# Performance work log

Measured on AMD Instinct MI355X. Metric: run time of the kernel, lower is better.

Reference implementation:

```python
import jax, jax.numpy as jnp
import numpy as np

BN_EPS = 1e-5


def setup_inputs() -> dict:
    key = jax.random.key(0)
    k_x, k_w, k_g, k_b, k_m, k_v = jax.random.split(key, 6)
    B, P, C = 8, 512, 1024
    x = jax.random.normal(k_x, (B, P, C), dtype=jnp.float32)
    # Linear(dim, dim, bias=False) weight, torch layout (out, in)
    W_qkv = jax.random.normal(k_w, (C, C), dtype=jnp.float32) * (1.0 / np.sqrt(C))
    # BatchNorm1d(dim) eval-mode params over channel axis
    bn_gamma = jnp.ones((C,), jnp.float32) + 0.01 * jax.random.normal(k_g, (C,), dtype=jnp.float32)
    bn_beta = 0.01 * jax.random.normal(k_b, (C,), dtype=jnp.float32)
    bn_mean = 0.01 * jax.random.normal(k_m, (C,), dtype=jnp.float32)
    bn_var = jnp.abs(1.0 + 0.01 * jax.random.normal(k_v, (C,), dtype=jnp.float32))
    gra_sharp = jnp.float32(2.0)
    return {"x": x, "W_qkv": W_qkv, "bn_gamma": bn_gamma, "bn_beta": bn_beta,
            "bn_mean": bn_mean, "bn_var": bn_var, "gra_sharp": gra_sharp}


def reference(x, W_qkv, bn_gamma, bn_beta, bn_mean, bn_var, gra_sharp):
    B, P, C = x.shape
    H = 8  # num_heads
    Wd = P // H  # per-head token width (heads split the SEQUENCE axis)

    # shared Linear(dim,dim,bias=False); q = k = v since same module on same x
    qkv = jnp.einsum('bpc,dc->bpd', x, W_qkv)          # (B, P, C)
    qkv = qkv.transpose(0, 2, 1)                        # (B, C, P)
    # BatchNorm1d(dim), eval mode: normalize channel axis (dim=1)
    inv = jax.lax.rsqrt(bn_var + BN_EPS)
    qkv = (qkv - bn_mean[None, :, None]) * (inv * bn_gamma)[None, :, None] + bn_beta[None, :, None]

    # split_last((H, -1)) on seq axis then transpose(1,2): (B, H, C, Wd)
    q = qkv.reshape(B, C, H, Wd).transpose(0, 2, 1, 3)
    k = q
    v = q

    # channel-by-channel scores per head: (B, H, C, C)
    scores = jnp.einsum('bhcw,bhdw->bhcd', q, k) / gra_sharp
    # NON-STANDARD: softmax over the HEAD axis (dim=1); dropout = identity (eval)
    attn = jax.nn.softmax(scores, axis=1)

    h = jnp.einsum('bhcd,bhdw->bhcw', attn, v)          # (B, H, C, Wd)
    h = h.transpose(0, 2, 1, 3).reshape(B, C, P)        # merge heads back into P
    h = h.transpose(0, 2, 1)                            # (B, P, C)
    return h, attn
```

## Files before the change

### kernel.cpp

```cpp
#include <hip/hip_runtime.h>
#include <math.h>

#define B 8
#define P 512
#define C 1024
#define H 8
#define WD 64
#define BN_EPS 1e-5f

typedef __attribute__((ext_vector_type(8))) __bf16 bf16x8;
typedef __attribute__((ext_vector_type(4))) __bf16 bf16x4;
typedef __attribute__((ext_vector_type(4))) float f32x4;

__global__ __launch_bounds__(256) void split_hi_lo(
    const float* __restrict__ x, const float* __restrict__ Wq,
    __bf16* __restrict__ xhi, __bf16* __restrict__ xlo,
    __bf16* __restrict__ whi, __bf16* __restrict__ wlo)
{
    const size_t NX4 = (size_t)B * P * C / 4;
    size_t idx = (size_t)blockIdx.x * 256 + threadIdx.x;
    float4 v;
    __bf16 *dh, *dl;
    size_t o;
    if (idx < NX4) {
        v = ((const float4*)x)[idx];
        dh = xhi; dl = xlo; o = idx * 4;
    } else {
        v = ((const float4*)Wq)[idx - NX4];
        dh = whi; dl = wlo; o = (idx - NX4) * 4;
    }
    float f[4] = {v.x, v.y, v.z, v.w};
    bf16x4 hv, lv;
    #pragma unroll
    for (int j = 0; j < 4; ++j) {
        __bf16 hb = (__bf16)f[j];
        hv[j] = hb;
        lv[j] = (__bf16)(f[j] - (float)hb);
    }
    *(bf16x4*)&dh[o] = hv;
    *(bf16x4*)&dl[o] = lv;
}

__global__ __launch_bounds__(256) void qkv_bn_mfma(
    const __bf16* __restrict__ xhi, const __bf16* __restrict__ xlo,
    const __bf16* __restrict__ whi, const __bf16* __restrict__ wlo,
    const float* __restrict__ gamma, const float* __restrict__ beta,
    const float* __restrict__ mean, const float* __restrict__ var,
    __bf16* __restrict__ Yhi, __bf16* __restrict__ Ylo, __bf16* __restrict__ Zhi)
{
    const int dt = blockIdx.x;
    const int pt = blockIdx.y;
    const int b  = blockIdx.z;
    const int t = threadIdx.x, lane = t & 63, wid = t >> 6;
    const int quadd = (wid >> 1) * 32, quadp = (wid & 1) * 32;
    const int lr = lane & 15, lk = (lane >> 4) * 8;

    const int drow0 = dt * 64 + quadd + lr;
    const size_t xrow0 = ((size_t)b * P + pt * 64 + quadp + lr) * C;

    f32x4 acc[2][2];
    #pragma unroll
    for (int tm = 0; tm < 2; ++tm)
        #pragma unroll
        for (int tn = 0; tn < 2; ++tn)
            acc[tm][tn] = (f32x4){0.f, 0.f, 0.f, 0.f};

    for (int c0 = 0; c0 < C; c0 += 32) {
        const int col = c0 + lk;
        bf16x8 ah[2], al[2], bh[2], bl[2];
        #pragma unroll
        for (int tm = 0; tm < 2; ++tm) {
            size_t ia = (size_t)(drow0 + tm * 16) * C + col;
            ah[tm] = *(const bf16x8*)&whi[ia];
            al[tm] = *(const bf16x8*)&wlo[ia];
        }
        #pragma unroll
        for (int tn = 0; tn < 2; ++tn) {
            size_t ib = xrow0 + (size_t)tn * 16 * C + col;
            bh[tn] = *(const bf16x8*)&xhi[ib];
            bl[tn] = *(const bf16x8*)&xlo[ib];
        }
        #pragma unroll
        for (int tm = 0; tm < 2; ++tm)
            #pragma unroll
            for (int tn = 0; tn < 2; ++tn) {
                acc[tm][tn] = __builtin_amdgcn_mfma_f32_16x16x32_bf16(ah[tm], bh[tn], acc[tm][tn], 0, 0, 0);
                acc[tm][tn] = __builtin_amdgcn_mfma_f32_16x16x32_bf16(ah[tm], bl[tn], acc[tm][tn], 0, 0, 0);
                acc[tm][tn] = __builtin_amdgcn_mfma_f32_16x16x32_bf16(al[tm], bh[tn], acc[tm][tn], 0, 0, 0);
            }
    }

    const int rgrp = (lane >> 4) * 4;
    #pragma unroll
    for (int tm = 0; tm < 2; ++tm) {
        const int dbase = dt * 64 + quadd + tm * 16 + rgrp;
        float4 g4 = *(const float4*)&gamma[dbase];
        float4 bb4 = *(const float4*)&beta[dbase];
        float4 m4 = *(const float4*)&mean[dbase];
        float4 v4 = *(const float4*)&var[dbase];
        float gf[4] = {g4.x, g4.y, g4.z, g4.w};
        float bf[4] = {bb4.x, bb4.y, bb4.z, bb4.w};
        float mf[4] = {m4.x, m4.y, m4.z, m4.w};
        float vf[4] = {v4.x, v4.y, v4.z, v4.w};
        float sc[4];
        #pragma unroll
        for (int r = 0; r < 4; ++r) sc[r] = rsqrtf(vf[r] + BN_EPS) * gf[r];

        #pragma unroll
        for (int tn = 0; tn < 2; ++tn) {
            const int p = pt * 64 + quadp + tn * 16 + lr;
            bf16x4 zq;
            #pragma unroll
            for (int r = 0; r < 4; ++r) {
                float n = (acc[tm][tn][r] - mf[r]) * sc[r] + bf[r];
                __bf16 hb = (__bf16)n;
                __bf16 lb = (__bf16)(n - (float)hb);
                size_t yi = ((size_t)b * C + dbase + r) * P + p;
                Yhi[yi] = hb;
                Ylo[yi] = lb;
                zq[r] = hb;
            }
            *(bf16x4*)&Zhi[((size_t)b * P + p) * C + dbase] = zq;
        }
    }
}

__global__ __launch_bounds__(256) void scores_softmax_mfma(
    const __bf16* __restrict__ Yhi, const __bf16* __restrict__ Ylo,
    const float* __restrict__ gs_ptr, float* __restrict__ attn)
{
    const int ct = blockIdx.x, dt = blockIdx.y, b = blockIdx.z;
    const int t = threadIdx.x, lane = t & 63, wid = t >> 6;
    const int quadc = (wid >> 1) * 32, quadd = (wid & 1) * 32;
    const int lr = lane & 15, lk = (lane >> 4) * 8;
    const float scale = 1.0f / gs_ptr[0];

    const size_t rowc = (size_t)b * C + ct * 64 + quadc + lr;
    const size_t rowd = (size_t)b * C + dt * 64 + quadd + lr;

    f32x4 acc[8][2][2];
    #pragma unroll
    for (int h = 0; h < H; ++h)
        #pragma unroll
        for (int tm = 0; tm < 2; ++tm)
            #pragma unroll
            for (int tn = 0; tn < 2; ++tn)
                acc[h][tm][tn] = (f32x4){0.f, 0.f, 0.f, 0.f};

    #pragma unroll
    for (int h = 0; h < H; ++h) {
        #pragma unroll
        for (int s = 0; s < 2; ++s) {
            const int col = h * 64 + s * 32 + lk;
            bf16x8 ah[2], al[2], bh[2], bl[2];
            #pragma unroll
            for (int tm = 0; tm < 2; ++tm) {
                size_t ia = (rowc + tm * 16) * P + col;
                ah[tm] = *(const bf16x8*)&Yhi[ia];
                al[tm] = *(const bf16x8*)&Ylo[ia];
                size_t ib = (rowd + tm * 16) * P + col;
                bh[tm] = *(const bf16x8*)&Yhi[ib];
                bl[tm] = *(const bf16x8*)&Ylo[ib];
            }
            #pragma unroll
            for (int tm = 0; tm < 2; ++tm)
                #pragma unroll
                for (int tn = 0; tn < 2; ++tn) {
                    acc[h][tm][tn] = __builtin_amdgcn_mfma_f32_16x16x32_bf16(ah[tm], bh[tn], acc[h][tm][tn], 0, 0, 0);
                    acc[h][tm][tn] = __builtin_amdgcn_mfma_f32_16x16x32_bf16(ah[tm], bl[tn], acc[h][tm][tn], 0, 0, 0);
                    acc[h][tm][tn] = __builtin_amdgcn_mfma_f32_16x16x32_bf16(al[tm], bh[tn], acc[h][tm][tn], 0, 0, 0);
                }
        }
    }

    #pragma unroll
    for (int tm = 0; tm < 2; ++tm)
        #pragma unroll
        for (int tn = 0; tn < 2; ++tn)
            #pragma unroll
            for (int r = 0; r < 4; ++r) {
                float v[8];
                float m = -1e30f;
                #pragma unroll
                for (int h = 0; h < H; ++h) {
                    v[h] = acc[h][tm][tn][r] * scale;
                    m = fmaxf(m, v[h]);
                }
                float ssum = 0.f;
                #pragma unroll
                for (int h = 0; h < H; ++h) { v[h] = __expf(v[h] - m); ssum += v[h]; }
                float inv = 1.0f / ssum;
                #pragma unroll
                for (int h = 0; h < H; ++h) acc[h][tm][tn][r] = v[h] * inv;
            }

    #pragma unroll
    for (int h = 0; h < H; ++h) {
        #pragma unroll
        for (int tm = 0; tm < 2; ++tm) {
            const int c = ct * 64 + quadc + tm * 16 + (lane >> 4) * 4;
            #pragma unroll
            for (int tn = 0; tn < 2; ++tn) {
                const int d = dt * 64 + quadd + tn * 16 + lr;
                float* op = attn + (((size_t)(b * H + h) * C + c) * C + d);
                #pragma unroll
                for (int r = 0; r < 4; ++r) op[(size_t)r * C] = acc[h][tm][tn][r];
            }
        }
    }
}

__global__ __launch_bounds__(256) void pv_mfma(
    const float* __restrict__ attn, const __bf16* __restrict__ Zhi,
    float* __restrict__ out0)
{
    const int ct = blockIdx.x;
    const int bh = blockIdx.y;
    const int b = bh >> 3, h = bh & 7;
    const int t = threadIdx.x, lane = t & 63, wid = t >> 6;
    const int quadc = (wid >> 1) * 64;
    const int quadw = (wid & 1) * 32;
    const int lr = lane & 15, lk = (lane >> 4) * 8;

    __shared__ __bf16 Ah[128 * 64];
    __shared__ __bf16 Al[128 * 64];

    const float* Ab = attn + ((size_t)bh * C + (size_t)ct * 128) * C;

    f32x4 acc[4][2];
    #pragma unroll
    for (int tm = 0; tm < 4; ++tm)
        #pragma unroll
        for (int tn = 0; tn < 2; ++tn)
            acc[tm][tn] = (f32x4){0.f, 0.f, 0.f, 0.f};

    const int sr  = t >> 4;
    const int scb = (t & 15) * 4;

    for (int d0 = 0; d0 < C; d0 += 64) {
        #pragma unroll
        for (int q = 0; q < 8; ++q) {
            int rr = sr + q * 16;
            float4 v = *(const float4*)&Ab[(size_t)rr * C + d0 + scb];
            __bf16 h0 = (__bf16)v.x, h1 = (__bf16)v.y, h2 = (__bf16)v.z, h3 = (__bf16)v.w;
            bf16x4 hq = {h0, h1, h2, h3};
            bf16x4 lq = {(__bf16)(v.x - (float)h0), (__bf16)(v.y - (float)h1),
                         (__bf16)(v.z - (float)h2), (__bf16)(v.w - (float)h3)};
            int off = (rr * 128 + scb * 2) ^ ((rr & 7) << 4);
            *(bf16x4*)((char*)Ah + off) = hq;
            *(bf16x4*)((char*)Al + off) = lq;
        }
        __syncthreads();
        #pragma unroll
        for (int s = 0; s < 2; ++s) {
            const int k0 = s * 32 + lk;
            bf16x8 bv[2];
            #pragma unroll
            for (int tn = 0; tn < 2; ++tn) {
                const int w = quadw + tn * 16 + lr;
                bv[tn] = *(const bf16x8*)&Zhi[((size_t)b * P + h * 64 + w) * C + d0 + k0];
            }
            #pragma unroll
            for (int tm = 0; tm < 4; ++tm) {
                const int row = quadc + tm * 16 + lr;
                const int off = (row * 128 + k0 * 2) ^ ((row & 7) << 4);
                bf16x8 a_h = *(const bf16x8*)((char*)Ah + off);
                bf16x8 a_l = *(const bf16x8*)((char*)Al + off);
                #pragma unroll
                for (int tn = 0; tn < 2; ++tn) {
                    acc[tm][tn] = __builtin_amdgcn_mfma_f32_16x16x32_bf16(a_h, bv[tn], acc[tm][tn], 0, 0, 0);
                    acc[tm][tn] = __builtin_amdgcn_mfma_f32_16x16x32_bf16(a_l, bv[tn], acc[tm][tn], 0, 0, 0);
                }
            }
        }
        __syncthreads();
    }

    #pragma unroll
    for (int tm = 0; tm < 4; ++tm) {
        const int c0 = ct * 128 + quadc + tm * 16 + (lane >> 4) * 4;
        #pragma unroll
        for (int tn = 0; tn < 2; ++tn) {
            const int w = quadw + tn * 16 + lr;
            f32x4 v = acc[tm][tn];
            *(f32x4*)&out0[((size_t)b * P + h * 64 + w) * C + c0] = v;
        }
    }
}

extern "C" void kernel_launch(void* const* d_in, const int* in_sizes, int n_in,
                              void* d_out, int out_size, void* d_ws, size_t ws_size,
                              hipStream_t stream) {
    const float* x     = (const float*)d_in[0];
    const float* Wq    = (const float*)d_in[1];
    const float* gamma = (const float*)d_in[2];
    const float* beta  = (const float*)d_in[3];
    const float* mean  = (const float*)d_in[4];
    const float* var   = (const float*)d_in[5];
    const float* gs    = (const float*)d_in[6];

    float* out0 = (float*)d_out;
    float* attn = (float*)d_out + (size_t)B * P * C;

    const size_t NE = (size_t)B * C * P;
    __bf16* Yhi = (__bf16*)d_ws;
    __bf16* Ylo = Yhi + NE;
    __bf16* Zhi = Ylo + NE;

    const size_t attn_elems = (size_t)B * H * C * C;
    __bf16* S = (__bf16*)(attn + (attn_elems - 5242880));
    __bf16* xhi = S;
    __bf16* xlo = xhi + (size_t)B * P * C;
    __bf16* whi = xlo + (size_t)B * P * C;
    __bf16* wlo = whi + (size_t)C * C;

    split_hi_lo<<<5120, 256, 0, stream>>>(x, Wq, xhi, xlo, whi, wlo);
    qkv_bn_mfma<<<dim3(16, 8, 8), 256, 0, stream>>>(xhi, xlo, whi, wlo,
                                                    gamma, beta, mean, var,
                                                    Yhi, Ylo, Zhi);
    scores_softmax_mfma<<<dim3(16, 16, 8), 256, 0, stream>>>(Yhi, Ylo, gs, attn);
    pv_mfma<<<dim3(8, 64), 256, 0, stream>>>(attn, Zhi, out0);
}
```

Measured before the change: 400.4 us.

## Fuse scores, head-axis softmax and PV product into one kernel

Merges the scores/softmax kernel and the PV kernel into a single kernel. Each block owns a 32-channel slice and loops over all d tiles: it computes the per-head scores, applies the head-axis softmax, writes attn, stages the probabilities as bf16 in LDS, and accumulates PV immediately. This removes the full fp32 re-read of the large attn tensor. The PV product now uses only the bf16 hi part of the probabilities instead of the hi+lo split, trading precision for fewer MFMAs. The grid shrinks to 256 blocks of 512 threads, and the partial sums are reduced across waves through LDS, which lowers occupancy and latency hiding.

```diff
diff --git a/kernel.cpp b/kernel.cpp
--- a/kernel.cpp
+++ b/kernel.cpp
@@ -5,7 +5,6 @@
 #define P 512
 #define C 1024
 #define H 8
-#define WD 64
 #define BN_EPS 1e-5f
 
 typedef __attribute__((ext_vector_type(8))) __bf16 bf16x8;
@@ -125,166 +124,138 @@
     }
 }
 
-__global__ __launch_bounds__(256) void scores_softmax_mfma(
+__global__ __launch_bounds__(512) void attn_fused(
     const __bf16* __restrict__ Yhi, const __bf16* __restrict__ Ylo,
-    const float* __restrict__ gs_ptr, float* __restrict__ attn)
-{
-    const int ct = blockIdx.x, dt = blockIdx.y, b = blockIdx.z;
-    const int t = threadIdx.x, lane = t & 63, wid = t >> 6;
-    const int quadc = (wid >> 1) * 32, quadd = (wid & 1) * 32;
-    const int lr = lane & 15, lk = (lane >> 4) * 8;
-    const float scale = 1.0f / gs_ptr[0];
-
-    const size_t rowc = (size_t)b * C + ct * 64 + quadc + lr;
-    const size_t rowd = (size_t)b * C + dt * 64 + quadd + lr;
-
-    f32x4 acc[8][2][2];
-    #pragma unroll
-    for (int h = 0; h < H; ++h)
-        #pragma unroll
-        for (int tm = 0; tm < 2; ++tm)
-            #pragma unroll
-            for (int tn = 0; tn < 2; ++tn)
-                acc[h][tm][tn] = (f32x4){0.f, 0.f, 0.f, 0.f};
-
-    #pragma unroll
-    for (int h = 0; h < H; ++h) {
-        #pragma unroll
-        for (int s = 0; s < 2; ++s) {
-            const int col = h * 64 + s * 32 + lk;
-            bf16x8 ah[2], al[2], bh[2], bl[2];
-            #pragma unroll
-            for (int tm = 0; tm < 2; ++tm) {
-                size_t ia = (rowc + tm * 16) * P + col;
-                ah[tm] = *(const bf16x8*)&Yhi[ia];
-                al[tm] = *(const bf16x8*)&Ylo[ia];
-                size_t ib = (rowd + tm * 16) * P + col;
-                bh[tm] = *(const bf16x8*)&Yhi[ib];
-                bl[tm] = *(const bf16x8*)&Ylo[ib];
-            }
-            #pragma unroll
-            for (int tm = 0; tm < 2; ++tm)
-                #pragma unroll
-                for (int tn = 0; tn < 2; ++tn) {
-                    acc[h][tm][tn] = __builtin_amdgcn_mfma_f32_16x16x32_bf16(ah[tm], bh[tn], acc[h][tm][tn], 0, 0, 0);
-                    acc[h][tm][tn] = __builtin_amdgcn_mfma_f32_16x16x32_bf16(ah[tm], bl[tn], acc[h][tm][tn], 0, 0, 0);
-                    acc[h][tm][tn] = __builtin_amdgcn_mfma_f32_16x16x32_bf16(al[tm], bh[tn], acc[h][tm][tn], 0, 0, 0);
-                }
-        }
-    }
-
-    #pragma unroll
-    for (int tm = 0; tm < 2; ++tm)
-        #pragma unroll
-        for (int tn = 0; tn < 2; ++tn)
-            #pragma unroll
-            for (int r = 0; r < 4; ++r) {
-                float v[8];
-                float m = -1e30f;
-                #pragma unroll
-                for (int h = 0; h < H; ++h) {
-                    v[h] = acc[h][tm][tn][r] * scale;
-                    m = fmaxf(m, v[h]);
-                }
-                float ssum = 0.f;
-                #pragma unroll
-                for (int h = 0; h < H; ++h) { v[h] = __expf(v[h] - m); ssum += v[h]; }
-                float inv = 1.0f / ssum;
-                #pragma unroll
-                for (int h = 0; h < H; ++h) acc[h][tm][tn][r] = v[h] * inv;
-            }
-
-    #pragma unroll
-    for (int h = 0; h < H; ++h) {
-        #pragma unroll
-        for (int tm = 0; tm < 2; ++tm) {
-            const int c = ct * 64 + quadc + tm * 16 + (lane >> 4) * 4;
-            #pragma unroll
-            for (int tn = 0; tn < 2; ++tn) {
-                const int d = dt * 64 + quadd + tn * 16 + lr;
-                float* op = attn + (((size_t)(b * H + h) * C + c) * C + d);
-                #pragma unroll
-                for (int r = 0; r < 4; ++r) op[(size_t)r * C] = acc[h][tm][tn][r];
-            }
-        }
-    }
-}
-
-__global__ __launch_bounds__(256) void pv_mfma(
-    const float* __restrict__ attn, const __bf16* __restrict__ Zhi,
-    float* __restrict__ out0)
+    const __bf16* __restrict__ Zhi, const float* __restrict__ gs_ptr,
+    float* __restrict__ attn, float* __restrict__ out0)
 {
     const int ct = blockIdx.x;
-    const int bh = blockIdx.y;
-    const int b = bh >> 3, h = bh & 7;
-    const int t = threadIdx.x, lane = t & 63, wid = t >> 6;
-    const int quadc = (wid >> 1) * 64;
-    const int quadw = (wid & 1) * 32;
-    const int lr = lane & 15, lk = (lane >> 4) * 8;
-
-    __shared__ __bf16 Ah[128 * 64];
-    __shared__ __bf16 Al[128 * 64];
-
-    const float* Ab = attn + ((size_t)bh * C + (size_t)ct * 128) * C;
-
-    f32x4 acc[4][2];
-    #pragma unroll
-    for (int tm = 0; tm < 4; ++tm)
-        #pragma unroll
-        for (int tn = 0; tn < 2; ++tn)
-            acc[tm][tn] = (f32x4){0.f, 0.f, 0.f, 0.f};
-
-    const int sr  = t >> 4;
-    const int scb = (t & 15) * 4;
-
-    for (int d0 = 0; d0 < C; d0 += 64) {
-        #pragma unroll
-        for (int q = 0; q < 8; ++q) {
-            int rr = sr + q * 16;
-            float4 v = *(const float4*)&Ab[(size_t)rr * C + d0 + scb];
-            __bf16 h0 = (__bf16)v.x, h1 = (__bf16)v.y, h2 = (__bf16)v.z, h3 = (__bf16)v.w;
-            bf16x4 hq = {h0, h1, h2, h3};
-            bf16x4 lq = {(__bf16)(v.x - (float)h0), (__bf16)(v.y - (float)h1),
-                         (__bf16)(v.z - (float)h2), (__bf16)(v.w - (float)h3)};
-            int off = (rr * 128 + scb * 2) ^ ((rr & 7) << 4);
-            *(bf16x4*)((char*)Ah + off) = hq;
-            *(bf16x4*)((char*)Al + off) = lq;
-        }
-        __syncthreads();
-        #pragma unroll
-        for (int s = 0; s < 2; ++s) {
-            const int k0 = s * 32 + lk;
-            bf16x8 bv[2];
+    const int b  = blockIdx.y;
+    const int c0 = ct * 32;
+    const int t = threadIdx.x, lane = t & 63, w = t >> 6;
+    const int lr = lane & 15, lk = (lane >> 4) * 8, rgrp = (lane >> 4) * 4;
+    const int si = w & 1;
+    const int sq = w >> 1;
+    const int pi = w & 1;
+    const int pj = (w >> 1) & 1;
+    const int pk = w >> 2;
+    const float scale = 1.0f / gs_ptr[0];
+
+    __shared__ __align__(16) char smem[65536];
+    __bf16 (*Plds)[32][72] = (__bf16(*)[32][72])smem;
+    float* Cmb = (float*)smem;
+    float (*Olds)[36] = (float(*)[36])smem;
+
+    f32x4 out_acc[8][2];
+    #pragma unroll
+    for (int h = 0; h < H; ++h) {
+        out_acc[h][0] = (f32x4){0.f, 0.f, 0.f, 0.f};
+        out_acc[h][1] = (f32x4){0.f, 0.f, 0.f, 0.f};
+    }
+
+    const int crow = c0 + si * 16 + lr;
+    const size_t YbaseC = ((size_t)b * C + crow) * P;
+
+    for (int dbase = 0; dbase < C; dbase += 64) {
+        const int drow = dbase + sq * 16 + lr;
+        const size_t YbaseD = ((size_t)b * C + drow) * P;
+
+        f32x4 sacc[8];
+        #pragma unroll
+        for (int h = 0; h < H; ++h) sacc[h] = (f32x4){0.f, 0.f, 0.f, 0.f};
+
+        #pragma unroll
+        for (int h = 0; h < H; ++h) {
+            #pragma unroll
+            for (int s = 0; s < 2; ++s) {
+                const int col = h * 64 + s * 32 + lk;
+                bf16x8 ah = *(const bf16x8*)&Yhi[YbaseC + col];
+                bf16x8 al = *(const bf16x8*)&Ylo[YbaseC + col];
+                bf16x8 bh = *(const bf16x8*)&Yhi[YbaseD + col];
+                bf16x8 bl = *(const bf16x8*)&Ylo[YbaseD + col];
+                sacc[h] = __builtin_amdgcn_mfma_f32_16x16x32_bf16(ah, bh, sacc[h], 0, 0, 0);
+                sacc[h] = __builtin_amdgcn_mfma_f32_16x16x32_bf16(ah, bl, sacc[h], 0, 0, 0);
+                sacc[h] = __builtin_amdgcn_mfma_f32_16x16x32_bf16(al, bh, sacc[h], 0, 0, 0);
+            }
+        }
+
+        const int dcol = dbase + sq * 16 + lr;
+        #pragma unroll
+        for (int r = 0; r < 4; ++r) {
+            const int c = c0 + si * 16 + rgrp + r;
+            float v[8];
+            float m = -1e30f;
+            #pragma unroll
+            for (int h = 0; h < H; ++h) {
+                v[h] = sacc[h][r] * scale;
+                m = fmaxf(m, v[h]);
+            }
+            float ssum = 0.f;
+            #pragma unroll
+            for (int h = 0; h < H; ++h) { v[h] = __expf(v[h] - m); ssum += v[h]; }
+            float inv = 1.0f / ssum;
+            #pragma unroll
+            for (int h = 0; h < H; ++h) {
+                float p = v[h] * inv;
+                attn[(((size_t)(b * H + h) * C + c) * C) + dcol] = p;
+                Plds[h][si * 16 + rgrp + r][sq * 16 + lr] = (__bf16)p;
+            }
+        }
+        __syncthreads();
+
+        #pragma unroll
+        for (int h = 0; h < H; ++h) {
+            bf16x8 a = *(const bf16x8*)&Plds[h][pi * 16 + lr][pk * 32 + lk];
             #pragma unroll
             for (int tn = 0; tn < 2; ++tn) {
-                const int w = quadw + tn * 16 + lr;
-                bv[tn] = *(const bf16x8*)&Zhi[((size_t)b * P + h * 64 + w) * C + d0 + k0];
-            }
-            #pragma unroll
-            for (int tm = 0; tm < 4; ++tm) {
-                const int row = quadc + tm * 16 + lr;
-                const int off = (row * 128 + k0 * 2) ^ ((row & 7) << 4);
-                bf16x8 a_h = *(const bf16x8*)((char*)Ah + off);
-                bf16x8 a_l = *(const bf16x8*)((char*)Al + off);
+                const int p = h * 64 + pj * 32 + tn * 16 + lr;
+                bf16x8 bv = *(const bf16x8*)&Zhi[((size_t)b * P + p) * C + dbase + pk * 32 + lk];
+                out_acc[h][tn] = __builtin_amdgcn_mfma_f32_16x16x32_bf16(a, bv, out_acc[h][tn], 0, 0, 0);
+            }
+        }
+        __syncthreads();
+    }
+
+    if (pk == 1) {
+        float* reg = Cmb + (size_t)(w - 4) * 4096;
+        #pragma unroll
+        for (int h = 0; h < H; ++h)
+            #pragma unroll
+            for (int tn = 0; tn < 2; ++tn)
                 #pragma unroll
-                for (int tn = 0; tn < 2; ++tn) {
-                    acc[tm][tn] = __builtin_amdgcn_mfma_f32_16x16x32_bf16(a_h, bv[tn], acc[tm][tn], 0, 0, 0);
-                    acc[tm][tn] = __builtin_amdgcn_mfma_f32_16x16x32_bf16(a_l, bv[tn], acc[tm][tn], 0, 0, 0);
-                }
-            }
-        }
-        __syncthreads();
-    }
-
-    #pragma unroll
-    for (int tm = 0; tm < 4; ++tm) {
-        const int c0 = ct * 128 + quadc + tm * 16 + (lane >> 4) * 4;
-        #pragma unroll
-        for (int tn = 0; tn < 2; ++tn) {
-            const int w = quadw + tn * 16 + lr;
-            f32x4 v = acc[tm][tn];
-            *(f32x4*)&out0[((size_t)b * P + h * 64 + w) * C + c0] = v;
-        }
+                for (int r = 0; r < 4; ++r)
+                    reg[((h * 2 + tn) * 4 + r) * 64 + lane] = out_acc[h][tn][r];
+    }
+    __syncthreads();
+    if (pk == 0) {
+        const float* reg = Cmb + (size_t)w * 4096;
+        #pragma unroll
+        for (int h = 0; h < H; ++h)
+            #pragma unroll
+            for (int tn = 0; tn < 2; ++tn)
+                #pragma unroll
+                for (int r = 0; r < 4; ++r)
+                    out_acc[h][tn][r] += reg[((h * 2 + tn) * 4 + r) * 64 + lane];
+    }
+    __syncthreads();
+
+    #pragma unroll
+    for (int h = 0; h < H; ++h) {
+        if (pk == 0) {
+            #pragma unroll
+            for (int tn = 0; tn < 2; ++tn)
+                #pragma unroll
+                for (int r = 0; r < 4; ++r)
+                    Olds[pj * 32 + tn * 16 + lr][pi * 16 + rgrp + r] = out_acc[h][tn][r];
+        }
+        __syncthreads();
+        {
+            const int row = t >> 3;
+            const int coff = (t & 7) * 4;
+            f32x4 vv = *(const f32x4*)&Olds[row][coff];
+            *(f32x4*)&out0[((size_t)b * P + h * 64 + row) * C + c0 + coff] = vv;
+        }
+        __syncthreads();
     }
 }
 
@@ -318,6 +289,5 @@
     qkv_bn_mfma<<<dim3(16, 8, 8), 256, 0, stream>>>(xhi, xlo, whi, wlo,
                                                     gamma, beta, mean, var,
                                                     Yhi, Ylo, Zhi);
-    scores_softmax_mfma<<<dim3(16, 16, 8), 256, 0, stream>>>(Yhi, Ylo, gs, attn);
-    pv_mfma<<<dim3(8, 64), 256, 0, stream>>>(attn, Zhi, out0);
-}
+    attn_fused<<<dim3(32, 8), 512, 0, stream>>>(Yhi, Ylo, Zhi, gs, attn, out0);
+}
```

After: 386.0 us. 1.04x faster.
